# Performance work log

Hardware: AMD Instinct MI355X
Metric: run time of the kernel (lower is better)

Reference implementation:

```python
import jax, jax.numpy as jnp
import numpy as np

B, L, D = 1, 2048, 2048
H, KV, HD = 32, 8, 64
REP = H // KV  # GQA repeat factor = 4


def _rope(t, cos, sin):
    # t: (B, L, nH, HD); cos/sin: (L, HD//2). Complex rotation on (even, odd) pairs.
    tr = t.reshape(*t.shape[:-1], HD // 2, 2)
    xr, xi = tr[..., 0], tr[..., 1]
    c = cos[None, :, None, :]
    s = sin[None, :, None, :]
    out_r = xr * c - xi * s
    out_i = xr * s + xi * c
    return jnp.stack([out_r, out_i], axis=-1).reshape(t.shape)


def setup_inputs() -> dict:
    key = jax.random.key(0)
    ks = jax.random.split(key, 5)
    x = jax.random.normal(ks[0], (B, L, D), jnp.float32)
    wq = jax.random.normal(ks[1], (D, H * HD), jnp.float32) * 0.02
    wk = jax.random.normal(ks[2], (D, KV * HD), jnp.float32) * 0.02
    wv = jax.random.normal(ks[3], (D, KV * HD), jnp.float32) * 0.02
    wo = jax.random.normal(ks[4], (H * HD, D), jnp.float32) * 0.02
    pos = jnp.arange(L, dtype=jnp.float32)
    inv_freq = 1.0 / (10000.0 ** (jnp.arange(0, HD, 2, dtype=jnp.float32) / HD))
    ang = pos[:, None] * inv_freq[None, :]  # (L, HD//2)
    freqs_cos = jnp.cos(ang)
    freqs_sin = jnp.sin(ang)
    # causal additive mask (L, L): 0 on/below diagonal, large negative above
    causal = jnp.arange(L)[None, :] <= jnp.arange(L)[:, None]
    mask = jnp.where(causal, 0.0, -1e9).astype(jnp.float32)
    return {"x": x, "wq": wq, "wk": wk, "wv": wv, "wo": wo,
            "freqs_cos": freqs_cos, "freqs_sin": freqs_sin, "mask": mask}


def reference(x, wq, wk, wv, wo, freqs_cos, freqs_sin, mask):
    q = (x @ wq).reshape(B, L, H, HD)
    k = (x @ wk).reshape(B, L, KV, HD)
    v = (x @ wv).reshape(B, L, KV, HD)
    q = _rope(q, freqs_cos, freqs_sin)
    k = _rope(k, freqs_cos, freqs_sin)
    # GQA: repeat_interleave kv heads
    k = jnp.repeat(k, REP, axis=2)
    v = jnp.repeat(v, REP, axis=2)
    # (B, nH, L, HD)
    q = q.transpose(0, 2, 1, 3)
    k = k.transpose(0, 2, 1, 3)
    v = v.transpose(0, 2, 1, 3)
    scores = jnp.einsum('bhqd,bhkd->bhqk', q, k) / np.float32(np.sqrt(HD))
    scores = scores + mask[None, None, :, :]
    attn = jax.nn.softmax(scores.astype(jnp.float32), axis=-1).astype(q.dtype)
    out = jnp.einsum('bhqk,bhkd->bqhd', attn, v).reshape(B, L, H * HD)
    return out @ wo
```

## Files before the change

kernel.cpp:

```cpp
#include <hip/hip_runtime.h>
#include <hip/hip_bf16.h>

#define L 2048
#define D 2048
#define NH 32
#define NKV 8
#define HD 64

typedef unsigned short u16;
typedef __attribute__((ext_vector_type(8))) short bf16x8;
typedef __attribute__((ext_vector_type(4))) float f32x4;

#define QSCALE 0.1803368801f

#define PANEL_OFF(d0, k) ((((size_t)((d0) >> 7) * 64 + ((k) >> 5)) << 12) + (((d0) & 127) << 5) + ((k) & 31))

__device__ __forceinline__ u16 f2bf(float x) {
    __hip_bfloat16 b = __float2bfloat16(x);
    return *reinterpret_cast<u16*>(&b);
}

__device__ __forceinline__ void gload_lds16(const void* g, void* l) {
    __builtin_amdgcn_global_load_lds(
        (const __attribute__((address_space(1))) unsigned int*)g,
        (__attribute__((address_space(3))) unsigned int*)l, 16, 0, 0);
}

__global__ __launch_bounds__(256) void prep_kernel(
    const float* __restrict__ x, u16* __restrict__ xb,
    const float* __restrict__ wq, const float* __restrict__ wk,
    const float* __restrict__ wv, const float* __restrict__ wo,
    u16* __restrict__ wqkvT, u16* __restrict__ woT)
{
    const int z = blockIdx.z;
    if (z == 4) {
        int i = (blockIdx.y * 64 + blockIdx.x) * 256 + threadIdx.x;
        int e = i * 4;
        int row = e >> 11, k0 = e & 2047;
        float4 v = ((const float4*)x)[i];
        ushort4 o;
        o.x = f2bf(v.x); o.y = f2bf(v.y); o.z = f2bf(v.z); o.w = f2bf(v.w);
        *(ushort4*)&xb[PANEL_OFF(row, k0)] = o;
        return;
    }
    const float* src; u16* dst; int C;
    if (z == 0)      { src = wq; dst = wqkvT;                           C = 2048; }
    else if (z == 1) { src = wk; dst = wqkvT + (size_t)2048 * 2048;     C = 512;  }
    else if (z == 2) { src = wv; dst = wqkvT + (size_t)2560 * 2048;     C = 512;  }
    else             { src = wo; dst = woT;                             C = 2048; }
    const int c0 = blockIdx.x * 32;
    if (c0 >= C) return;
    const int r0 = blockIdx.y * 32;
    __shared__ float tile[32][33];
    const int tx = threadIdx.x & 31, ty = threadIdx.x >> 5;
#pragma unroll
    for (int i = 0; i < 32; i += 8)
        tile[ty + i][tx] = src[(size_t)(r0 + ty + i) * C + c0 + tx];
    __syncthreads();
#pragma unroll
    for (int i = 0; i < 32; i += 8) {
        const int n = c0 + ty + i, k = r0 + tx;
        dst[PANEL_OFF(n, k)] = f2bf(tile[tx][ty + i]);
    }
}

#define VT_LDS 72

template <int MODE>
__global__ __launch_bounds__(256) void gemm4w_kernel(
    const u16* __restrict__ A, const u16* __restrict__ Bt, void* __restrict__ Cout,
    int N, int K, const float* __restrict__ fc, const float* __restrict__ fs,
    u16* __restrict__ vt)
{
    __shared__ __align__(16) u16 As[4][128 * 32];
    __shared__ __align__(16) u16 Bs[4][128 * 32];
    const int tid = threadIdx.x;
    const int w = tid >> 6, lane = tid & 63;

    const int nwg = (int)(gridDim.x * gridDim.y);
    int bid = (int)blockIdx.y * (int)gridDim.x + (int)blockIdx.x;
    bid = (bid & 7) * (nwg >> 3) + (bid >> 3);
    const int m0 = (bid / (int)gridDim.x) * 128, n0 = (bid % (int)gridDim.x) * 128;

    const int l15 = lane & 15, quad = lane >> 4, q8 = quad * 8;
    const int wr = (w >> 1) * 64, wc = (w & 1) * 64;
    const int l8 = lane * 8;
    const int wch = w * 1024;

    const u16* pa = A  + ((size_t)(m0 >> 7) * (K / 32) << 12);
    const u16* pb = Bt + ((size_t)(n0 >> 7) * (K / 32) << 12);

    f32x4 acc[4][4];
#pragma unroll
    for (int i = 0; i < 4; ++i)
#pragma unroll
        for (int j = 0; j < 4; ++j) acc[i][j] = (f32x4){0.f, 0.f, 0.f, 0.f};

    const int nSub = K / 32;
    const int nOut = nSub / 2;
#pragma unroll
    for (int s = 0; s < 4; ++s) {
        const size_t so = (size_t)s << 12;
        gload_lds16(pa + so + wch + l8,       &As[s][wch]);
        gload_lds16(pa + so + wch + 512 + l8, &As[s][wch + 512]);
        gload_lds16(pb + so + wch + l8,       &Bs[s][wch]);
        gload_lds16(pb + so + wch + 512 + l8, &Bs[s][wch + 512]);
    }
    for (int it = 0; it < nOut; ++it) {
        const int s0 = 2 * it, cb0 = s0 & 3, cb1 = (s0 + 1) & 3;
        asm volatile("s_waitcnt vmcnt(8)" ::: "memory");
        asm volatile("s_barrier" ::: "memory");
        bf16x8 a0[4], a1[4], b0[4], b1[4];
#pragma unroll
        for (int t = 0; t < 4; ++t) {
            a0[t] = *(const bf16x8*)&As[cb0][(wr + t * 16 + l15) * 32 + q8];
            b0[t] = *(const bf16x8*)&Bs[cb0][(wc + t * 16 + l15) * 32 + q8];
            a1[t] = *(const bf16x8*)&As[cb1][(wr + t * 16 + l15) * 32 + q8];
            b1[t] = *(const bf16x8*)&Bs[cb1][(wc + t * 16 + l15) * 32 + q8];
        }
        asm volatile("s_waitcnt lgkmcnt(0)" ::: "memory");
        asm volatile("s_barrier" ::: "memory");
        {
            const int sp0 = s0 + 4, sp1 = s0 + 5;
            const size_t k0 = (size_t)((sp0 < nSub) ? sp0 : 0) << 12;
            const size_t k1 = (size_t)((sp1 < nSub) ? sp1 : 0) << 12;
            gload_lds16(pa + k0 + wch + l8,       &As[cb0][wch]);
            gload_lds16(pa + k0 + wch + 512 + l8, &As[cb0][wch + 512]);
            gload_lds16(pb + k0 + wch + l8,       &Bs[cb0][wch]);
            gload_lds16(pb + k0 + wch + 512 + l8, &Bs[cb0][wch + 512]);
            gload_lds16(pa + k1 + wch + l8,       &As[cb1][wch]);
            gload_lds16(pa + k1 + wch + 512 + l8, &As[cb1][wch + 512]);
            gload_lds16(pb + k1 + wch + l8,       &Bs[cb1][wch]);
            gload_lds16(pb + k1 + wch + 512 + l8, &Bs[cb1][wch + 512]);
        }
#pragma unroll
        for (int i = 0; i < 4; ++i)
#pragma unroll
            for (int j = 0; j < 4; ++j) {
                acc[i][j] = __builtin_amdgcn_mfma_f32_16x16x32_bf16(a0[i], b0[j], acc[i][j], 0, 0, 0);
                acc[i][j] = __builtin_amdgcn_mfma_f32_16x16x32_bf16(a1[i], b1[j], acc[i][j], 0, 0, 0);
            }
    }

    if (MODE == 0) {
        float* C = (float*)Cout;
#pragma unroll
        for (int i = 0; i < 4; ++i)
#pragma unroll
            for (int j = 0; j < 4; ++j)
#pragma unroll
                for (int r = 0; r < 4; ++r)
                    C[(size_t)(m0 + wr + i * 16 + quad * 4 + r) * N + n0 + wc + j * 16 + l15] = acc[i][j][r];
    } else {
        __syncthreads();
        u16* O = (u16*)Cout;
        const int vc0 = n0 + wc;
        if (vc0 < 2560) {
            const float scl = (vc0 < 2048) ? QSCALE : 1.0f;
            const int odd = l15 & 1;
#pragma unroll
            for (int i = 0; i < 4; ++i)
#pragma unroll
                for (int j = 0; j < 4; ++j)
#pragma unroll
                    for (int r = 0; r < 4; ++r) {
                        const int row = m0 + wr + i * 16 + quad * 4 + r;
                        const int col = vc0 + j * 16 + l15;
                        float v = acc[i][j][r];
                        const int i2 = (j * 16 + l15) >> 1;
                        const float c = fc[row * 32 + i2], s = fs[row * 32 + i2];
                        const float p = __shfl_xor(v, 1);
                        float o = (odd ? (p * s + v * c) : (v * c - p * s)) * scl;
                        O[(size_t)row * 3072 + col] = f2bf(o);
                    }
        } else {
            u16* ws_ = (w < 2 ? (u16*)As : (u16*)Bs) + (w & 1) * (64 * VT_LDS);
#pragma unroll
            for (int i = 0; i < 4; ++i)
#pragma unroll
                for (int j = 0; j < 4; ++j)
#pragma unroll
                    for (int r = 0; r < 4; ++r)
                        ws_[(j * 16 + l15) * VT_LDS + i * 16 + quad * 4 + r] = f2bf(acc[i][j][r]);
#pragma unroll
            for (int t = 0; t < 8; ++t) {
                const int vr = t * 8 + (lane >> 3);
                const int c8 = (lane & 7) * 8;
                bf16x8 vv = *(const bf16x8*)&ws_[vr * VT_LDS + c8];
                *(bf16x8*)&vt[(size_t)(vc0 - 2560 + vr) * 2048 + m0 + wr + c8] = vv;
            }
        }
    }
}

#define ATT_LDP 72

__global__ __launch_bounds__(256) void attn_mfma_kernel(
    const u16* __restrict__ qkv,
    const u16* __restrict__ vt,
    u16* __restrict__ ab)
{
    __shared__ __align__(16) u16 Ks[2][64 * 64];
    __shared__ __align__(16) u16 Vs[2][64 * 64];
    __shared__ __align__(16) u16 Ps[4][16 * ATT_LDP];

    const int h = blockIdx.x;
    const int tile = (int)gridDim.y - 1 - (int)blockIdx.y;
    const int gkv = h >> 2;
    const int tid = threadIdx.x;
    const int w = tid >> 6, lane = tid & 63;
    const int l15 = lane & 15, quad = lane >> 4;
    const int q0 = tile * 64 + w * 16;

    const int srow = lane >> 3, schunk = lane & 7;
    const int r0_ = w * 16 + srow, r1_ = w * 16 + 8 + srow;
    const int c0_ = (schunk ^ (r0_ & 7)) * 8, c1_ = (schunk ^ (r1_ & 7)) * 8;
    const u16* kbase = qkv + 2048 + gkv * HD;
    const u16* vbase = vt + (size_t)gkv * HD * 2048;

    bf16x8 ones;
#pragma unroll
    for (int j = 0; j < 8; ++j) ones[j] = (short)0x3F80;

    bf16x8 qa[2];
    {
        const u16* qrow = qkv + (size_t)(q0 + l15) * 3072 + h * HD + quad * 8;
        qa[0] = *(const bf16x8*)(qrow);
        qa[1] = *(const bf16x8*)(qrow + 32);
    }
    f32x4 O[4];
#pragma unroll
    for (int i = 0; i < 4; ++i) O[i] = (f32x4){0.f, 0.f, 0.f, 0.f};
    float m_run[4], l_run[4];
#pragma unroll
    for (int r = 0; r < 4; ++r) { m_run[r] = -1e30f; l_run[r] = 0.f; }

    gload_lds16(kbase + (size_t)r0_ * 3072 + c0_,        &Ks[0][(w * 16) * 64]);
    gload_lds16(kbase + (size_t)r1_ * 3072 + c1_,        &Ks[0][(w * 16 + 8) * 64]);
    gload_lds16(vbase + (size_t)r0_ * 2048 + c0_,        &Vs[0][(w * 16) * 64]);
    gload_lds16(vbase + (size_t)r1_ * 2048 + c1_,        &Vs[0][(w * 16 + 8) * 64]);

    for (int c = 0; c <= tile; ++c) {
        const int cb = c & 1, nb = cb ^ 1;
        const int kn = (c < tile ? c + 1 : tile) * 64;
        gload_lds16(kbase + (size_t)(kn + r0_) * 3072 + c0_, &Ks[nb][(w * 16) * 64]);
        gload_lds16(kbase + (size_t)(kn + r1_) * 3072 + c1_, &Ks[nb][(w * 16 + 8) * 64]);
        gload_lds16(vbase + (size_t)r0_ * 2048 + kn + c0_,   &Vs[nb][(w * 16) * 64]);
        gload_lds16(vbase + (size_t)r1_ * 2048 + kn + c1_,   &Vs[nb][(w * 16 + 8) * 64]);
        asm volatile("s_waitcnt vmcnt(4)" ::: "memory");
        asm volatile("s_barrier" ::: "memory");

        f32x4 S[4];
        __builtin_amdgcn_s_setprio(1);
#pragma unroll
        for (int kt = 0; kt < 4; ++kt) {
            const int kr = kt * 16 + l15, kx = (kr & 7);
            bf16x8 b0 = *(const bf16x8*)&Ks[cb][kr * 64 + ((quad ^ kx) * 8)];
            bf16x8 b1 = *(const bf16x8*)&Ks[cb][kr * 64 + (((quad + 4) ^ kx) * 8)];
            f32x4 s = (f32x4){0.f, 0.f, 0.f, 0.f};
            s = __builtin_amdgcn_mfma_f32_16x16x32_bf16(qa[0], b0, s, 0, 0, 0);
            s = __builtin_amdgcn_mfma_f32_16x16x32_bf16(qa[1], b1, s, 0, 0, 0);
            S[kt] = s;
        }
        __builtin_amdgcn_s_setprio(0);
        if (c == tile) {
#pragma unroll
            for (int kt = 0; kt < 4; ++kt) {
                int keyl = kt * 16 + l15;
#pragma unroll
                for (int r = 0; r < 4; ++r)
                    if (keyl > w * 16 + quad * 4 + r) S[kt][r] = -1e30f;
            }
        }
        float alpha[4];
#pragma unroll
        for (int r = 0; r < 4; ++r) {
            float mx = fmaxf(fmaxf(S[0][r], S[1][r]), fmaxf(S[2][r], S[3][r]));
#pragma unroll
            for (int off = 1; off < 16; off <<= 1) mx = fmaxf(mx, __shfl_xor(mx, off));
            float mn = fmaxf(m_run[r], mx);
            alpha[r] = exp2f(m_run[r] - mn);
            m_run[r] = mn;
#pragma unroll
            for (int kt = 0; kt < 4; ++kt) S[kt][r] = exp2f(S[kt][r] - mn);
        }
        u16* pw = Ps[w];
#pragma unroll
        for (int kt = 0; kt < 4; ++kt)
#pragma unroll
            for (int r = 0; r < 4; ++r)
                pw[(quad * 4 + r) * ATT_LDP + kt * 16 + l15] = f2bf(S[kt][r]);
        bf16x8 pa0 = *(const bf16x8*)&pw[l15 * ATT_LDP + quad * 8];
        bf16x8 pa1 = *(const bf16x8*)&pw[l15 * ATT_LDP + 32 + quad * 8];

        f32x4 rs = (f32x4){0.f, 0.f, 0.f, 0.f};
        rs = __builtin_amdgcn_mfma_f32_16x16x32_bf16(pa0, ones, rs, 0, 0, 0);
        rs = __builtin_amdgcn_mfma_f32_16x16x32_bf16(pa1, ones, rs, 0, 0, 0);
#pragma unroll
        for (int r = 0; r < 4; ++r) l_run[r] = l_run[r] * alpha[r] + rs[r];

#pragma unroll
        for (int dt = 0; dt < 4; ++dt)
#pragma unroll
            for (int r = 0; r < 4; ++r) O[dt][r] *= alpha[r];
        __builtin_amdgcn_s_setprio(1);
#pragma unroll
        for (int dt = 0; dt < 4; ++dt) {
            const int vr = dt * 16 + l15, vx = (vr & 7);
            bf16x8 b0 = *(const bf16x8*)&Vs[cb][vr * 64 + ((quad ^ vx) * 8)];
            bf16x8 b1 = *(const bf16x8*)&Vs[cb][vr * 64 + (((quad + 4) ^ vx) * 8)];
            O[dt] = __builtin_amdgcn_mfma_f32_16x16x32_bf16(pa0, b0, O[dt], 0, 0, 0);
            O[dt] = __builtin_amdgcn_mfma_f32_16x16x32_bf16(pa1, b1, O[dt], 0, 0, 0);
        }
        __builtin_amdgcn_s_setprio(0);
        asm volatile("s_barrier" ::: "memory");
    }
#pragma unroll
    for (int r = 0; r < 4; ++r) {
        float inv = 1.0f / l_run[r];
        const int q = q0 + quad * 4 + r;
        const int pbase = ((q >> 7) << 18) + ((q & 127) << 5);
#pragma unroll
        for (int dt = 0; dt < 4; ++dt) {
            const int col = h * HD + dt * 16 + l15;
            ab[pbase + ((col >> 5) << 12) + (col & 31)] = f2bf(O[dt][r] * inv);
        }
    }
}

extern "C" void kernel_launch(void* const* d_in, const int* in_sizes, int n_in,
                              void* d_out, int out_size, void* d_ws, size_t ws_size,
                              hipStream_t stream)
{
    const float* x  = (const float*)d_in[0];
    const float* wq = (const float*)d_in[1];
    const float* wk = (const float*)d_in[2];
    const float* wv = (const float*)d_in[3];
    const float* wo = (const float*)d_in[4];
    const float* fc = (const float*)d_in[5];
    const float* fs = (const float*)d_in[6];
    float* out = (float*)d_out;

    u16* xb     = (u16*)d_ws;
    u16* wqkvT  = xb     + (size_t)2048 * 2048;
    u16* woT    = wqkvT  + (size_t)3072 * 2048;
    u16* qkv_bf = woT    + (size_t)2048 * 2048;
    u16* vt     = qkv_bf + (size_t)2048 * 3072;
    u16* ab     = vt     + (size_t)512 * 2048;

    prep_kernel<<<dim3(64, 64, 5), 256, 0, stream>>>(x, xb, wq, wk, wv, wo, wqkvT, woT);

    gemm4w_kernel<1><<<dim3(3072 / 128, 2048 / 128), 256, 0, stream>>>(
        xb, wqkvT, qkv_bf, 3072, 2048, fc, fs, vt);

    attn_mfma_kernel<<<dim3(NH, L / 64), 256, 0, stream>>>(qkv_bf, vt, ab);

    gemm4w_kernel<0><<<dim3(2048 / 128, 2048 / 128), 256, 0, stream>>>(
        ab, woT, out, 2048, 2048, nullptr, nullptr, nullptr);
}
```

Measured before the change: 249.8 us.

## Compute transposed scores to keep P in registers and skip rescaling lazily

The QK^T MFMA operands are swapped so each lane holds the scores for a single query column. The softmax row max and sum then need only two cross-quad shuffles, and P can be packed to bf16 in registers and fed straight into 16x16x16 MFMAs for PV, with no round trip through LDS and no ones-vector MFMA for the row sum. A lazy rescale is added: the running max and O are updated only when some lane's new max exceeds the old one by more than 8 (log2 units). This saves exp and multiply work but lets unnormalised exponents grow to about 2^8, and PV now uses twice as many smaller MFMAs plus shuffles to map per-query factors back onto O's row layout.

Result: no change. 245.3 us (-1.8%).

```diff
diff --git a/kernel.cpp b/kernel.cpp
--- a/kernel.cpp
+++ b/kernel.cpp
@@ -9,9 +9,14 @@
 
 typedef unsigned short u16;
 typedef __attribute__((ext_vector_type(8))) short bf16x8;
+typedef __attribute__((ext_vector_type(4))) short bf16x4;
 typedef __attribute__((ext_vector_type(4))) float f32x4;
 
 #define QSCALE 0.1803368801f
+
+__device__ __forceinline__ f32x4 mfma16(bf16x4 a, bf16x4 b, f32x4 c) {
+    return __builtin_amdgcn_mfma_f32_16x16x16bf16_1k(a, b, c, 0, 0, 0);
+}
 
 #define PANEL_OFF(d0, k) ((((size_t)((d0) >> 7) * 64 + ((k) >> 5)) << 12) + (((d0) & 127) << 5) + ((k) & 31))
 
@@ -193,8 +198,6 @@
     }
 }
 
-#define ATT_LDP 72
-
 __global__ __launch_bounds__(256) void attn_mfma_kernel(
     const u16* __restrict__ qkv,
     const u16* __restrict__ vt,
@@ -202,7 +205,6 @@
 {
     __shared__ __align__(16) u16 Ks[2][64 * 64];
     __shared__ __align__(16) u16 Vs[2][64 * 64];
-    __shared__ __align__(16) u16 Ps[4][16 * ATT_LDP];
 
     const int h = blockIdx.x;
     const int tile = (int)gridDim.y - 1 - (int)blockIdx.y;
@@ -218,10 +220,6 @@
     const u16* kbase = qkv + 2048 + gkv * HD;
     const u16* vbase = vt + (size_t)gkv * HD * 2048;
 
-    bf16x8 ones;
-#pragma unroll
-    for (int j = 0; j < 8; ++j) ones[j] = (short)0x3F80;
-
     bf16x8 qa[2];
     {
         const u16* qrow = qkv + (size_t)(q0 + l15) * 3072 + h * HD + quad * 8;
@@ -231,14 +229,13 @@
     f32x4 O[4];
 #pragma unroll
     for (int i = 0; i < 4; ++i) O[i] = (f32x4){0.f, 0.f, 0.f, 0.f};
-    float m_run[4], l_run[4];
-#pragma unroll
-    for (int r = 0; r < 4; ++r) { m_run[r] = -1e30f; l_run[r] = 0.f; }
-
-    gload_lds16(kbase + (size_t)r0_ * 3072 + c0_,        &Ks[0][(w * 16) * 64]);
-    gload_lds16(kbase + (size_t)r1_ * 3072 + c1_,        &Ks[0][(w * 16 + 8) * 64]);
-    gload_lds16(vbase + (size_t)r0_ * 2048 + c0_,        &Vs[0][(w * 16) * 64]);
-    gload_lds16(vbase + (size_t)r1_ * 2048 + c1_,        &Vs[0][(w * 16 + 8) * 64]);
+    float m_run = -1e30f;
+    float l_run = 0.f;
+
+    gload_lds16(kbase + (size_t)r0_ * 3072 + c0_, &Ks[0][(w * 16) * 64]);
+    gload_lds16(kbase + (size_t)r1_ * 3072 + c1_, &Ks[0][(w * 16 + 8) * 64]);
+    gload_lds16(vbase + (size_t)r0_ * 2048 + c0_, &Vs[0][(w * 16) * 64]);
+    gload_lds16(vbase + (size_t)r1_ * 2048 + c1_, &Vs[0][(w * 16 + 8) * 64]);
 
     for (int c = 0; c <= tile; ++c) {
         const int cb = c & 1, nb = cb ^ 1;
@@ -250,74 +247,86 @@
         asm volatile("s_waitcnt vmcnt(4)" ::: "memory");
         asm volatile("s_barrier" ::: "memory");
 
-        f32x4 S[4];
+        f32x4 s[4];
         __builtin_amdgcn_s_setprio(1);
 #pragma unroll
         for (int kt = 0; kt < 4; ++kt) {
             const int kr = kt * 16 + l15, kx = (kr & 7);
             bf16x8 b0 = *(const bf16x8*)&Ks[cb][kr * 64 + ((quad ^ kx) * 8)];
             bf16x8 b1 = *(const bf16x8*)&Ks[cb][kr * 64 + (((quad + 4) ^ kx) * 8)];
-            f32x4 s = (f32x4){0.f, 0.f, 0.f, 0.f};
-            s = __builtin_amdgcn_mfma_f32_16x16x32_bf16(qa[0], b0, s, 0, 0, 0);
-            s = __builtin_amdgcn_mfma_f32_16x16x32_bf16(qa[1], b1, s, 0, 0, 0);
-            S[kt] = s;
+            f32x4 t = (f32x4){0.f, 0.f, 0.f, 0.f};
+            t = __builtin_amdgcn_mfma_f32_16x16x32_bf16(b0, qa[0], t, 0, 0, 0);
+            t = __builtin_amdgcn_mfma_f32_16x16x32_bf16(b1, qa[1], t, 0, 0, 0);
+            s[kt] = t;
         }
         __builtin_amdgcn_s_setprio(0);
         if (c == tile) {
 #pragma unroll
-            for (int kt = 0; kt < 4; ++kt) {
-                int keyl = kt * 16 + l15;
+            for (int kt = 0; kt < 4; ++kt)
 #pragma unroll
                 for (int r = 0; r < 4; ++r)
-                    if (keyl > w * 16 + quad * 4 + r) S[kt][r] = -1e30f;
+                    if (kt * 16 + quad * 4 + r > w * 16 + l15) s[kt][r] = -1e30f;
+        }
+        float mx = fmaxf(fmaxf(fmaxf(s[0][0], s[0][1]), fmaxf(s[0][2], s[0][3])),
+                         fmaxf(fmaxf(s[1][0], s[1][1]), fmaxf(s[1][2], s[1][3])));
+        mx = fmaxf(mx, fmaxf(fmaxf(fmaxf(s[2][0], s[2][1]), fmaxf(s[2][2], s[2][3])),
+                             fmaxf(fmaxf(s[3][0], s[3][1]), fmaxf(s[3][2], s[3][3]))));
+        mx = fmaxf(mx, __shfl_xor(mx, 16));
+        mx = fmaxf(mx, __shfl_xor(mx, 32));
+        const bool resc = !__all(mx <= m_run + 8.f);
+        float aL = 1.f;
+        if (resc) {
+            const float mn = fmaxf(m_run, mx);
+            aL = exp2f(m_run - mn);
+            m_run = mn;
+        }
+#pragma unroll
+        for (int kt = 0; kt < 4; ++kt)
+#pragma unroll
+            for (int r = 0; r < 4; ++r) s[kt][r] = exp2f(s[kt][r] - m_run);
+        float rsum = 0.f;
+#pragma unroll
+        for (int kt = 0; kt < 4; ++kt)
+#pragma unroll
+            for (int r = 0; r < 4; ++r) rsum += s[kt][r];
+        rsum += __shfl_xor(rsum, 16);
+        rsum += __shfl_xor(rsum, 32);
+        l_run = resc ? (l_run * aL + rsum) : (l_run + rsum);
+        bf16x4 pbf[4];
+#pragma unroll
+        for (int kt = 0; kt < 4; ++kt) {
+            unsigned int lo, hi;
+            asm("v_cvt_pk_bf16_f32 %0, %1, %2" : "=v"(lo) : "v"(s[kt][0]), "v"(s[kt][1]));
+            asm("v_cvt_pk_bf16_f32 %0, %1, %2" : "=v"(hi) : "v"(s[kt][2]), "v"(s[kt][3]));
+            union { unsigned int u[2]; bf16x4 v; } cv;
+            cv.u[0] = lo; cv.u[1] = hi;
+            pbf[kt] = cv.v;
+        }
+        if (resc) {
+#pragma unroll
+            for (int r = 0; r < 4; ++r) {
+                const float aQ = __shfl(aL, (quad << 4) + (quad << 2) + r);
+                O[0][r] *= aQ; O[1][r] *= aQ; O[2][r] *= aQ; O[3][r] *= aQ;
             }
         }
-        float alpha[4];
-#pragma unroll
-        for (int r = 0; r < 4; ++r) {
-            float mx = fmaxf(fmaxf(S[0][r], S[1][r]), fmaxf(S[2][r], S[3][r]));
-#pragma unroll
-            for (int off = 1; off < 16; off <<= 1) mx = fmaxf(mx, __shfl_xor(mx, off));
-            float mn = fmaxf(m_run[r], mx);
-            alpha[r] = exp2f(m_run[r] - mn);
-            m_run[r] = mn;
-#pragma unroll
-            for (int kt = 0; kt < 4; ++kt) S[kt][r] = exp2f(S[kt][r] - mn);
-        }
-        u16* pw = Ps[w];
-#pragma unroll
-        for (int kt = 0; kt < 4; ++kt)
-#pragma unroll
-            for (int r = 0; r < 4; ++r)
-                pw[(quad * 4 + r) * ATT_LDP + kt * 16 + l15] = f2bf(S[kt][r]);
-        bf16x8 pa0 = *(const bf16x8*)&pw[l15 * ATT_LDP + quad * 8];
-        bf16x8 pa1 = *(const bf16x8*)&pw[l15 * ATT_LDP + 32 + quad * 8];
-
-        f32x4 rs = (f32x4){0.f, 0.f, 0.f, 0.f};
-        rs = __builtin_amdgcn_mfma_f32_16x16x32_bf16(pa0, ones, rs, 0, 0, 0);
-        rs = __builtin_amdgcn_mfma_f32_16x16x32_bf16(pa1, ones, rs, 0, 0, 0);
-#pragma unroll
-        for (int r = 0; r < 4; ++r) l_run[r] = l_run[r] * alpha[r] + rs[r];
-
-#pragma unroll
-        for (int dt = 0; dt < 4; ++dt)
-#pragma unroll
-            for (int r = 0; r < 4; ++r) O[dt][r] *= alpha[r];
         __builtin_amdgcn_s_setprio(1);
 #pragma unroll
         for (int dt = 0; dt < 4; ++dt) {
             const int vr = dt * 16 + l15, vx = (vr & 7);
-            bf16x8 b0 = *(const bf16x8*)&Vs[cb][vr * 64 + ((quad ^ vx) * 8)];
-            bf16x8 b1 = *(const bf16x8*)&Vs[cb][vr * 64 + (((quad + 4) ^ vx) * 8)];
-            O[dt] = __builtin_amdgcn_mfma_f32_16x16x32_bf16(pa0, b0, O[dt], 0, 0, 0);
-            O[dt] = __builtin_amdgcn_mfma_f32_16x16x32_bf16(pa1, b1, O[dt], 0, 0, 0);
+#pragma unroll
+            for (int kt = 0; kt < 4; ++kt) {
+                bf16x4 vf = *(const bf16x4*)&Vs[cb][vr * 64 +
+                    (((2 * kt + (quad >> 1)) ^ vx) << 3) + ((quad & 1) << 2)];
+                O[dt] = mfma16(pbf[kt], vf, O[dt]);
+            }
         }
         __builtin_amdgcn_s_setprio(0);
         asm volatile("s_barrier" ::: "memory");
     }
 #pragma unroll
     for (int r = 0; r < 4; ++r) {
-        float inv = 1.0f / l_run[r];
+        const float lq = __shfl(l_run, (quad << 4) + (quad << 2) + r);
+        const float inv = 1.0f / lq;
         const int q = q0 + quad * 4 + r;
         const int pbase = ((q >> 7) << 18) + ((q & 127) << 5);
 #pragma unroll
```
